# Optimization experiments

Hardware: AMD Instinct MI355X
Metric: run time of the kernel (lower is better)

## Reference

```python
import jax, jax.numpy as jnp
import numpy as np

B, N, M, K, D, DO = 4, 32768, 8192, 16, 128, 128


def setup_inputs() -> dict:
    key = jax.random.key(0)
    ks = jax.random.split(key, 8)
    return dict(
        xyz=jax.random.normal(ks[0], (B, N, 3), jnp.float32),
        x=jax.random.normal(ks[1], (B, D, N), jnp.float32),
        xyz_center=jax.random.normal(ks[2], (B, M, 3), jnp.float32),
        idx=jax.random.randint(ks[3], (B, M, K), 0, N, jnp.int32),
        alpha=jnp.ones((1,), jnp.float32),
        beta=jnp.ones((1,), jnp.float32),
        norm_radius=jnp.ones((1,), jnp.float32),
        w1=jax.random.normal(ks[4], (K, 3), jnp.float32) * 0.1,
        g1=jnp.ones((K,), jnp.float32),
        b1=jnp.zeros((K,), jnp.float32),
        w2=jax.random.normal(ks[5], (K, 2 * K), jnp.float32) * 0.1,
        g2=jnp.ones((K,), jnp.float32),
        b2=jnp.zeros((K,), jnp.float32),
        w3=jax.random.normal(ks[6], (K, 2 * K), jnp.float32) * 0.1,
        cv_w=jax.random.normal(ks[7], (DO, D, K), jnp.float32) * 0.02,
    )


def _inorm(t, g, b, eps=1e-5):
    # InstanceNorm2d: normalize each (batch, channel) plane over spatial dims (m, k)
    mu = t.mean(axis=(2, 3), keepdims=True)
    var = t.var(axis=(2, 3), keepdims=True)
    return (t - mu) * jax.lax.rsqrt(var + eps) * g[None, :, None, None] + b[None, :, None, None]


def reference(xyz, x, xyz_center, idx, alpha, beta, norm_radius, w1, g1, b1, w2, g2, b2, w3, cv_w):
    k = idx.shape[-1]
    gather = jax.vmap(lambda pts, i: pts[i])  # per-batch gather
    xyz_group = gather(xyz, idx)                      # b m k 3
    x_group = gather(jnp.swapaxes(x, 1, 2), idx)      # b m k d

    pts = xyz_group - xyz_center[:, :, None, :]       # b m k 3
    # dist computed on detached pts (torch .detach())
    dist = jnp.sqrt(jnp.sum(jnp.square(jax.lax.stop_gradient(pts)), -1))  # b m k
    mean_radius = dist.max(-1).mean()
    nr = norm_radius * 0.9 + mean_radius * 0.1        # EMA-updated radius (non-trainable)
    pts = pts / nr

    dw = jax.nn.sigmoid(-alpha * dist + beta)         # b m k
    s = dw.sum(-1, keepdims=True)
    s = s + (s == 0).astype(dw.dtype) + 1e-6
    dw = dw / s * k
    dw4 = dw[:, None, :, :]                           # b 1 m k

    ptsT = jnp.transpose(pts, (0, 3, 1, 2))           # b 3 m k
    mat = jax.nn.relu(_inorm(jnp.einsum('bcmk,oc->bomk', ptsT, w1), g1, b1))
    mp1 = jnp.broadcast_to((mat * dw4).max(-1, keepdims=True), mat.shape)
    mat = jax.nn.relu(_inorm(jnp.einsum('bcmk,oc->bomk', jnp.concatenate([mat, mp1], 1), w2), g2, b2))
    mp2 = jnp.broadcast_to((mat * dw4).max(-1, keepdims=True), mat.shape)
    mat = jax.nn.relu(jnp.einsum('bcmk,oc->bomk', jnp.concatenate([mat, mp2], 1), w3)) * dw4

    out = jnp.einsum('bmkd,bjmk->bdmj', x_group, mat)  # b d m k
    out = jnp.einsum('bdmj,odj->bom', out, cv_w)
    return out
```

## Files before the change

### kernel.cpp

```cpp
#include <hip/hip_runtime.h>
#include <hip/hip_bf16.h>

#define BB 4
#define NN 32768
#define MM 8192
#define KK 16
#define DD 128
#define DOUT 128
#define TT 2048

typedef unsigned short ushortT;
typedef unsigned int uintT;
typedef __attribute__((ext_vector_type(8))) short short8;
typedef __attribute__((ext_vector_type(4))) float f32x4;
typedef __attribute__((ext_vector_type(2))) float f32x2;

__device__ __forceinline__ ushortT f2bf(float f) {
  union { float f; uintT u; } v; v.f = f;
  uintT u = v.u;
  return (ushortT)((u + 0x7FFFu + ((u >> 16) & 1u)) >> 16);
}

#define ST_MAXD 0
#define ST_E1 16
#define ST_A1 160
#define ST_B1 224
#define ST_E2 288
#define ST_A2 416
#define ST_B2 480

__global__ __launch_bounds__(256) void kxT(const float* __restrict__ x, ushortT* __restrict__ xTb) {
  __shared__ float tile[32][33];
  const int b = blockIdx.z;
  const int n0 = blockIdx.x * 32, d0 = blockIdx.y * 32;
  const int tx = threadIdx.x, ty = threadIdx.y;
  const float* xp = x + (size_t)b * DD * NN;
  #pragma unroll
  for (int i = 0; i < 4; i++)
    tile[ty + i * 8][tx] = xp[(size_t)(d0 + ty + i * 8) * NN + n0 + tx];
  __syncthreads();
  ushortT* op = xTb + (size_t)b * NN * DD;
  #pragma unroll
  for (int i = 0; i < 4; i++)
    op[(size_t)(n0 + ty + i * 8) * DD + d0 + tx] = f2bf(tile[tx][ty + i * 8]);
}

__global__ __launch_bounds__(256) void kWb(const float* __restrict__ cw, ushortT* __restrict__ wb) {
  const int i = blockIdx.x * 256 + threadIdx.x;
  wb[i] = f2bf(cw[i]);
}

__global__ __launch_bounds__(256) void kpassA(const float* __restrict__ xyz,
    const float* __restrict__ xyzc, const int* __restrict__ idx,
    const float* __restrict__ w1, float* __restrict__ st, float4* __restrict__ pts4) {
  const int b = blockIdx.y;
  const int tid = threadIdx.x;
  const int mloc = tid >> 4, k = tid & 15;
  const int m = blockIdx.x * 16 + mloc;
  const int gi = (b * MM + m) * KK + k;
  const int n = idx[gi];
  const float cx = xyzc[(b * MM + m) * 3 + 0];
  const float cy = xyzc[(b * MM + m) * 3 + 1];
  const float cz = xyzc[(b * MM + m) * 3 + 2];
  const float* p = xyz + ((size_t)b * NN + n) * 3;
  const float px = p[0] - cx, py = p[1] - cy, pz = p[2] - cz;
  const float dist = sqrtf(px * px + py * py + pz * pz);
  pts4[gi] = (float4){px, py, pz, dist};
  float maxd = dist;
  maxd = fmaxf(maxd, __shfl_xor(maxd, 1));
  maxd = fmaxf(maxd, __shfl_xor(maxd, 2));
  maxd = fmaxf(maxd, __shfl_xor(maxd, 4));
  maxd = fmaxf(maxd, __shfl_xor(maxd, 8));
  __shared__ float red[16];
  __shared__ float wred[4][32];
  if (k == 0) red[mloc] = maxd;
  float vs[16], vq[16];
  #pragma unroll
  for (int o = 0; o < 16; o++) {
    float e = px * w1[3 * o] + py * w1[3 * o + 1] + pz * w1[3 * o + 2];
    vs[o] = e; vq[o] = e * e;
  }
  #pragma unroll
  for (int s = 1; s < 64; s <<= 1) {
    #pragma unroll
    for (int o = 0; o < 16; o++) {
      vs[o] += __shfl_xor(vs[o], s);
      vq[o] += __shfl_xor(vq[o], s);
    }
  }
  const int wv = tid >> 6, lane = tid & 63;
  if (lane == 0) {
    #pragma unroll
    for (int o = 0; o < 16; o++) { wred[wv][o] = vs[o]; wred[wv][16 + o] = vq[o]; }
  }
  __syncthreads();
  if (tid < 32) {
    float a = wred[0][tid] + wred[1][tid] + wred[2][tid] + wred[3][tid];
    atomicAdd(&st[ST_E1 + b * 32 + tid], a);
  }
  if (tid == 0) {
    float s = 0.f;
    #pragma unroll
    for (int i = 0; i < 16; i++) s += red[i];
    atomicAdd(&st[ST_MAXD], s);
  }
}

__global__ void kS1(const float* __restrict__ nrad, const float* __restrict__ g1,
                    const float* __restrict__ b1, float* __restrict__ st) {
  const int tid = threadIdx.x;
  if (tid >= 64) return;
  const float meanrad = st[ST_MAXD] / (float)(BB * MM);
  const float nr = nrad[0] * 0.9f + meanrad * 0.1f;
  const int b = tid >> 4, o = tid & 15;
  const float cnt = (float)(MM * KK);
  const float sum = st[ST_E1 + b * 32 + o];
  const float sq  = st[ST_E1 + b * 32 + 16 + o];
  const float mu = sum / cnt;
  float var = sq / cnt - mu * mu; var = fmaxf(var, 0.f);
  const float invs = rsqrtf(var + 1e-5f * nr * nr);
  const float a = invs * g1[o];
  st[ST_A1 + b * 16 + o] = a;
  st[ST_B1 + b * 16 + o] = b1[o] - mu * a;
}

__global__ __launch_bounds__(256) void kpassB(const float4* __restrict__ pts4,
    const float* __restrict__ alpha, const float* __restrict__ beta,
    const float* __restrict__ w1, const float* __restrict__ w2,
    float* __restrict__ st) {
  const int b = blockIdx.y;
  const int tid = threadIdx.x;
  __shared__ float wred[4][32];
  const int gi = b * MM * KK + blockIdx.x * 256 + tid;
  const float4 p4 = pts4[gi];
  const float px = p4.x, py = p4.y, pz = p4.z, dist = p4.w;
  float dwv = 1.f / (1.f + expf(alpha[0] * dist - beta[0]));
  float s = dwv;
  s += __shfl_xor(s, 1); s += __shfl_xor(s, 2); s += __shfl_xor(s, 4); s += __shfl_xor(s, 8);
  s = s + (s == 0.f ? 1.f : 0.f) + 1e-6f;
  dwv = dwv / s * 16.f;
  f32x2 v1[16];
  #pragma unroll
  for (int o = 0; o < 16; o++) {
    float e = px * w1[3 * o] + py * w1[3 * o + 1] + pz * w1[3 * o + 2];
    float v = e * st[ST_A1 + b * 16 + o] + st[ST_B1 + b * 16 + o];
    v = fmaxf(v, 0.f);
    float t = v * dwv;
    t = fmaxf(t, __shfl_xor(t, 1)); t = fmaxf(t, __shfl_xor(t, 2));
    t = fmaxf(t, __shfl_xor(t, 4)); t = fmaxf(t, __shfl_xor(t, 8));
    if (o & 1) { v1[o >> 1].y = v; v1[8 + (o >> 1)].y = t; }
    else       { v1[o >> 1].x = v; v1[8 + (o >> 1)].x = t; }
  }
  float vs[16], vq[16];
  #pragma unroll
  for (int o = 0; o < 16; o++) {
    f32x2 acc = {0.f, 0.f};
    #pragma unroll
    for (int cp = 0; cp < 16; cp++) {
      const f32x2 wv = *(const f32x2*)(w2 + o * 32 + 2 * cp);
      acc += v1[cp] * wv;
    }
    const float e = acc.x + acc.y;
    vs[o] = e; vq[o] = e * e;
  }
  #pragma unroll
  for (int s2 = 1; s2 < 64; s2 <<= 1) {
    #pragma unroll
    for (int o = 0; o < 16; o++) {
      vs[o] += __shfl_xor(vs[o], s2);
      vq[o] += __shfl_xor(vq[o], s2);
    }
  }
  const int wv = tid >> 6, lane = tid & 63;
  if (lane == 0) {
    #pragma unroll
    for (int o = 0; o < 16; o++) { wred[wv][o] = vs[o]; wred[wv][16 + o] = vq[o]; }
  }
  __syncthreads();
  if (tid < 32) {
    float a = wred[0][tid] + wred[1][tid] + wred[2][tid] + wred[3][tid];
    atomicAdd(&st[ST_E2 + b * 32 + tid], a);
  }
}

__global__ void kS2(const float* __restrict__ g2, const float* __restrict__ b2,
                    float* __restrict__ st) {
  const int tid = threadIdx.x;
  if (tid >= 64) return;
  const int b = tid >> 4, o = tid & 15;
  const float cnt = (float)(MM * KK);
  const float sum = st[ST_E2 + b * 32 + o];
  const float sq  = st[ST_E2 + b * 32 + 16 + o];
  const float mu = sum / cnt;
  float var = sq / cnt - mu * mu; var = fmaxf(var, 0.f);
  const float invs = rsqrtf(var + 1e-5f);
  const float a = invs * g2[o];
  st[ST_A2 + b * 16 + o] = a;
  st[ST_B2 + b * 16 + o] = b2[o] - mu * a;
}

__global__ __launch_bounds__(256, 6) void kMat3(const float* __restrict__ xyz,
    const float* __restrict__ xyzc, const int* __restrict__ idx,
    const float* __restrict__ alpha, const float* __restrict__ beta,
    const float* __restrict__ w1, const float* __restrict__ w2,
    const float* __restrict__ w3, const float* __restrict__ st,
    float* __restrict__ mat3g) {
  const int b = blockIdx.y;
  const int tid = threadIdx.x;
  const int mloc = tid >> 4, k1 = tid & 15;
  const int m = blockIdx.x * 16 + mloc;
  const int gi = (b * MM + m) * KK + k1;
  const int n = idx[gi];
  const float cx = xyzc[(b * MM + m) * 3 + 0];
  const float cy = xyzc[(b * MM + m) * 3 + 1];
  const float cz = xyzc[(b * MM + m) * 3 + 2];
  const float* p = xyz + ((size_t)b * NN + n) * 3;
  const float px = p[0] - cx, py = p[1] - cy, pz = p[2] - cz;
  const float dist = sqrtf(px * px + py * py + pz * pz);
  float dwv = 1.f / (1.f + expf(alpha[0] * dist - beta[0]));
  {
    float s = dwv;
    s += __shfl_xor(s, 1); s += __shfl_xor(s, 2); s += __shfl_xor(s, 4); s += __shfl_xor(s, 8);
    s = s + (s == 0.f ? 1.f : 0.f) + 1e-6f;
    dwv = dwv / s * 16.f;
  }
  f32x2 v1[16];
  #pragma unroll
  for (int o = 0; o < 16; o++) {
    float e = px * w1[3 * o] + py * w1[3 * o + 1] + pz * w1[3 * o + 2];
    float v = e * st[ST_A1 + b * 16 + o] + st[ST_B1 + b * 16 + o];
    v = fmaxf(v, 0.f);
    float t = v * dwv;
    t = fmaxf(t, __shfl_xor(t, 1)); t = fmaxf(t, __shfl_xor(t, 2));
    t = fmaxf(t, __shfl_xor(t, 4)); t = fmaxf(t, __shfl_xor(t, 8));
    if (o & 1) { v1[o >> 1].y = v; v1[8 + (o >> 1)].y = t; }
    else       { v1[o >> 1].x = v; v1[8 + (o >> 1)].x = t; }
  }
  float in2[16];
  #pragma unroll
  for (int o = 0; o < 16; o++) {
    f32x2 acc = {0.f, 0.f};
    #pragma unroll
    for (int cp = 0; cp < 16; cp++) {
      const f32x2 wv = *(const f32x2*)(w2 + o * 32 + 2 * cp);
      acc += v1[cp] * wv;
    }
    float v = (acc.x + acc.y) * st[ST_A2 + b * 16 + o] + st[ST_B2 + b * 16 + o];
    in2[o] = fmaxf(v, 0.f);
  }
  f32x2 v2[16];
  #pragma unroll
  for (int o = 0; o < 16; o++) {
    float t = in2[o] * dwv;
    t = fmaxf(t, __shfl_xor(t, 1)); t = fmaxf(t, __shfl_xor(t, 2));
    t = fmaxf(t, __shfl_xor(t, 4)); t = fmaxf(t, __shfl_xor(t, 8));
    if (o & 1) { v2[o >> 1].y = in2[o]; v2[8 + (o >> 1)].y = t; }
    else       { v2[o >> 1].x = in2[o]; v2[8 + (o >> 1)].x = t; }
  }
  float m3v[16];
  #pragma unroll
  for (int j = 0; j < 16; j++) {
    f32x2 acc = {0.f, 0.f};
    #pragma unroll
    for (int cp = 0; cp < 16; cp++) {
      const f32x2 wv = *(const f32x2*)(w3 + j * 32 + 2 * cp);
      acc += v2[cp] * wv;
    }
    m3v[j] = fmaxf(acc.x + acc.y, 0.f) * dwv;
  }
  const int swz1 = (k1 ^ (k1 >> 2)) & 3;
  float* m3w = mat3g + (((size_t)b * MM + blockIdx.x * 16) << 8) + tid * 16;
  #pragma unroll
  for (int q = 0; q < 4; q++)
    *(f32x4*)(m3w + ((q ^ swz1) << 2)) =
        (f32x4){m3v[4 * q], m3v[4 * q + 1], m3v[4 * q + 2], m3v[4 * q + 3]};
}

__global__ __launch_bounds__(512, 3) void kF2(const int* __restrict__ idx,
    const float* __restrict__ mat3g, const ushortT* __restrict__ xTb,
    ushortT* __restrict__ Aout) {
  __shared__ float mat3s[32 * 256];
  const int b = blockIdx.y;
  const int tid = threadIdx.x;
  const int m0 = blockIdx.x * 32;

  const int wid = __builtin_amdgcn_readfirstlane(tid >> 6);
  const int lane = tid & 63;
  const int mh = lane >> 5;
  const int dq = lane & 31;
  const int d0 = dq * 4;
  const ushortT* xb = xTb + (size_t)b * NN * DD + d0;

  uint2 xA[16], xB[16];

#define PREF(dst, gg) do {                                                 \
    const int* ib0 = idx + ((b * MM + m0 + (gg) * 16 + wid * 2) << 4);     \
    const int* ib1 = ib0 + 16;                                             \
    _Pragma("unroll")                                                      \
    for (int t = 0; t < 16; t++) {                                         \
      const int ke = ib0[t], ko = ib1[t];                                  \
      const uintT nn = (uintT)(mh ? ko : ke);                              \
      (dst)[t] = *(const uint2*)(xb + ((size_t)nn << 7));                  \
    }                                                                      \
  } while (0)

  PREF(xA, 0);

  {
    const f32x4* src = (const f32x4*)(mat3g + (((size_t)b * MM + m0) << 8));
    f32x4* dst = (f32x4*)mat3s;
    #pragma unroll
    for (int i = 0; i < 4; i++)
      dst[tid + i * 512] = src[tid + i * 512];
  }
  __syncthreads();

#define COMP(src, gg) do {                                                 \
    const float* m3base = &mat3s[((gg) * 16 + wid * 2 + mh) * 256];        \
    f32x2 a2[4][8];                                                        \
    _Pragma("unroll")                                                      \
    for (int d = 0; d < 4; d++)                                            \
      _Pragma("unroll")                                                    \
      for (int c = 0; c < 8; c++) a2[d][c] = (f32x2){0.f, 0.f};            \
    _Pragma("unroll")                                                      \
    for (int t = 0; t < 16; t++) {                                         \
      const int sw = (t ^ (t >> 2)) & 3;                                   \
      const uint2 xv = (src)[t];                                           \
      const f32x4 mq0 = *(const f32x4*)(m3base + t * 16 + ((0 ^ sw) << 2));\
      const f32x4 mq1 = *(const f32x4*)(m3base + t * 16 + ((1 ^ sw) << 2));\
      const f32x4 mq2 = *(const f32x4*)(m3base + t * 16 + ((2 ^ sw) << 2));\
      const f32x4 mq3 = *(const f32x4*)(m3base + t * 16 + ((3 ^ sw) << 2));\
      float xs[4];                                                         \
      xs[0] = __uint_as_float(xv.x << 16);                                 \
      xs[1] = __uint_as_float(xv.x & 0xFFFF0000u);                         \
      xs[2] = __uint_as_float(xv.y << 16);                                 \
      xs[3] = __uint_as_float(xv.y & 0xFFFF0000u);                         \
      f32x2 mp[8];                                                         \
      mp[0] = mq0.lo; mp[1] = mq0.hi;                                      \
      mp[2] = mq1.lo; mp[3] = mq1.hi;                                      \
      mp[4] = mq2.lo; mp[5] = mq2.hi;                                      \
      mp[6] = mq3.lo; mp[7] = mq3.hi;                                      \
      _Pragma("unroll")                                                    \
      for (int d = 0; d < 4; d++) {                                        \
        const float xd = xs[d];                                            \
        _Pragma("unroll")                                                  \
        for (int c = 0; c < 8; c++)                                        \
          a2[d][c] += mp[c] * xd;                                          \
      }                                                                    \
    }                                                                      \
    ushortT* aop = Aout + ((size_t)b * MM + m0 + (gg) * 16 + wid * 2 + mh) * TT + d0 * 16; \
    _Pragma("unroll")                                                      \
    for (int d = 0; d < 4; d++) {                                          \
      uintT u[8];                                                          \
      _Pragma("unroll")                                                    \
      for (int c = 0; c < 8; c++)                                          \
        u[c] = (uintT)f2bf(a2[d][c].x) | ((uintT)f2bf(a2[d][c].y) << 16);  \
      *(uint4*)(aop + d * 16)     = (uint4){u[0], u[1], u[2], u[3]};       \
      *(uint4*)(aop + d * 16 + 8) = (uint4){u[4], u[5], u[6], u[7]};       \
    }                                                                      \
  } while (0)

  PREF(xB, 1);
  COMP(xA, 0);
  COMP(xB, 1);

#undef PREF
#undef COMP
}

__global__ __launch_bounds__(512) void kgemm(const ushortT* __restrict__ Wb,
                                             const ushortT* __restrict__ Aout,
                                             float* __restrict__ out) {
  __shared__ ushortT At[128 * 40];
  __shared__ ushortT Bt[128 * 40];
  const int b = blockIdx.y;
  const int m0 = blockIdx.x * 128;
  const int tid = threadIdx.x;
  const int w = tid >> 6, l = tid & 63;
  const int ow = (w >> 2) * 64, mw = (w & 3) * 32;
  const int fr = l & 15, fg = l >> 4;
  f32x4 acc[4][2];
  #pragma unroll
  for (int i = 0; i < 4; i++)
    #pragma unroll
    for (int j = 0; j < 2; j++)
      acc[i][j] = (f32x4){0.f, 0.f, 0.f, 0.f};
  const int srow = tid >> 2, sk = (tid & 3) * 8;
  const ushortT* wp = Wb + srow * TT + sk;
  const ushortT* ap = Aout + ((size_t)b * MM + m0 + srow) * TT + sk;
  for (int k0 = 0; k0 < TT; k0 += 32) {
    uint4 wv = *(const uint4*)(wp + k0);
    uint4 av = *(const uint4*)(ap + k0);
    *(uint4*)&At[srow * 40 + sk] = wv;
    *(uint4*)&Bt[srow * 40 + sk] = av;
    __syncthreads();
    short8 a[4], bfrag[2];
    #pragma unroll
    for (int i = 0; i < 4; i++) a[i] = *(short8*)&At[(ow + i * 16 + fr) * 40 + fg * 8];
    #pragma unroll
    for (int j = 0; j < 2; j++) bfrag[j] = *(short8*)&Bt[(mw + j * 16 + fr) * 40 + fg * 8];
    #pragma unroll
    for (int i = 0; i < 4; i++)
      #pragma unroll
      for (int j = 0; j < 2; j++)
        acc[i][j] = __builtin_amdgcn_mfma_f32_16x16x32_bf16(a[i], bfrag[j], acc[i][j], 0, 0, 0);
    __syncthreads();
  }
  #pragma unroll
  for (int i = 0; i < 4; i++)
    #pragma unroll
    for (int j = 0; j < 2; j++)
      #pragma unroll
      for (int r = 0; r < 4; r++) {
        const int o = ow + i * 16 + fg * 4 + r;
        const int m = m0 + mw + j * 16 + fr;
        out[((size_t)b * DOUT + o) * MM + m] = acc[i][j][r];
      }
}

#define XTB_OFF 0
#define PTS_OFF 33554432
#define MAT3_OFF 33554432
#define AOUT_OFF 67108864
#define WB_OFF 201326592
#define ST_OFF 201850880

extern "C" void kernel_launch(void* const* d_in, const int* in_sizes, int n_in,
                              void* d_out, int out_size, void* d_ws, size_t ws_size,
                              hipStream_t stream) {
  const float* xyz  = (const float*)d_in[0];
  const float* x    = (const float*)d_in[1];
  const float* xyzc = (const float*)d_in[2];
  const int*   idx  = (const int*)d_in[3];
  const float* alpha = (const float*)d_in[4];
  const float* beta  = (const float*)d_in[5];
  const float* nrad  = (const float*)d_in[6];
  const float* w1 = (const float*)d_in[7];
  const float* g1 = (const float*)d_in[8];
  const float* b1 = (const float*)d_in[9];
  const float* w2 = (const float*)d_in[10];
  const float* g2 = (const float*)d_in[11];
  const float* b2 = (const float*)d_in[12];
  const float* w3 = (const float*)d_in[13];
  const float* cvw = (const float*)d_in[14];
  char* ws = (char*)d_ws;
  ushortT* xTb  = (ushortT*)(ws + XTB_OFF);
  float4*  pts4 = (float4*)(ws + PTS_OFF);
  float*   mat3g = (float*)(ws + MAT3_OFF);
  ushortT* Aout = (ushortT*)(ws + AOUT_OFF);
  ushortT* Wb   = (ushortT*)(ws + WB_OFF);
  float*   st   = (float*)(ws + ST_OFF);
  float* out = (float*)d_out;

  hipMemsetAsync(st, 0, 4096, stream);
  kxT<<<dim3(NN / 32, DD / 32, BB), dim3(32, 8), 0, stream>>>(x, xTb);
  kWb<<<dim3(DOUT * TT / 256), 256, 0, stream>>>(cvw, Wb);
  kpassA<<<dim3(MM / 16, BB), 256, 0, stream>>>(xyz, xyzc, idx, w1, st, pts4);
  kS1<<<1, 64, 0, stream>>>(nrad, g1, b1, st);
  kpassB<<<dim3(MM / 16, BB), 256, 0, stream>>>(pts4, alpha, beta, w1, w2, st);
  kS2<<<1, 64, 0, stream>>>(g2, b2, st);
  kMat3<<<dim3(MM / 16, BB), 256, 0, stream>>>(xyz, xyzc, idx, alpha, beta, w1, w2, w3, st, mat3g);
  kF2<<<dim3(MM / 32, BB), 512, 0, stream>>>(idx, mat3g, xTb, Aout);
  kgemm<<<dim3(MM / 128, BB), 512, 0, stream>>>(Wb, Aout, out);
}
```

Before: 236.2 us.

## Fuse mat3 MLP computation into gather-aggregate kernel via shared memory

Merges the kernel that computed the per-neighbor MLP weights (mat3) with the kernel that gathers features and aggregates them. mat3 now goes straight to LDS instead of being written to and read back from a global workspace, and the kernel reads precomputed pts4 (offsets plus distance) instead of re-gathering xyz. This removes one launch and the global round-trip of the mat3 buffer. In exchange, blocks shrink to 256 threads over 16 centers with lower occupancy hints, and the feature prefetch now overlaps with MLP compute, which raises register pressure.

```diff
diff --git a/kernel.cpp b/kernel.cpp
--- a/kernel.cpp
+++ b/kernel.cpp
@@ -199,24 +199,20 @@
   st[ST_B2 + b * 16 + o] = b2[o] - mu * a;
 }
 
-__global__ __launch_bounds__(256, 6) void kMat3(const float* __restrict__ xyz,
-    const float* __restrict__ xyzc, const int* __restrict__ idx,
+__global__ __launch_bounds__(256, 3) void kF1m(const float4* __restrict__ pts4,
+    const int* __restrict__ idx,
     const float* __restrict__ alpha, const float* __restrict__ beta,
-    const float* __restrict__ w1, const float* __restrict__ w2,
-    const float* __restrict__ w3, const float* __restrict__ st,
-    float* __restrict__ mat3g) {
+    const float* __restrict__ w1, const float* __restrict__ w2, const float* __restrict__ w3,
+    const float* __restrict__ st, const ushortT* __restrict__ xTb, ushortT* __restrict__ Aout) {
+  __shared__ float mat3s[16 * 256];
   const int b = blockIdx.y;
   const int tid = threadIdx.x;
+  const int m0 = blockIdx.x * 16;
+
   const int mloc = tid >> 4, k1 = tid & 15;
-  const int m = blockIdx.x * 16 + mloc;
-  const int gi = (b * MM + m) * KK + k1;
-  const int n = idx[gi];
-  const float cx = xyzc[(b * MM + m) * 3 + 0];
-  const float cy = xyzc[(b * MM + m) * 3 + 1];
-  const float cz = xyzc[(b * MM + m) * 3 + 2];
-  const float* p = xyz + ((size_t)b * NN + n) * 3;
-  const float px = p[0] - cx, py = p[1] - cy, pz = p[2] - cz;
-  const float dist = sqrtf(px * px + py * py + pz * pz);
+  const int gi = (b * MM + m0) * KK + tid;
+  const float4 p4 = pts4[gi];
+  const float px = p4.x, py = p4.y, pz = p4.z, dist = p4.w;
   float dwv = 1.f / (1.f + expf(alpha[0] * dist - beta[0]));
   {
     float s = dwv;
@@ -236,53 +232,6 @@
     if (o & 1) { v1[o >> 1].y = v; v1[8 + (o >> 1)].y = t; }
     else       { v1[o >> 1].x = v; v1[8 + (o >> 1)].x = t; }
   }
-  float in2[16];
-  #pragma unroll
-  for (int o = 0; o < 16; o++) {
-    f32x2 acc = {0.f, 0.f};
-    #pragma unroll
-    for (int cp = 0; cp < 16; cp++) {
-      const f32x2 wv = *(const f32x2*)(w2 + o * 32 + 2 * cp);
-      acc += v1[cp] * wv;
-    }
-    float v = (acc.x + acc.y) * st[ST_A2 + b * 16 + o] + st[ST_B2 + b * 16 + o];
-    in2[o] = fmaxf(v, 0.f);
-  }
-  f32x2 v2[16];
-  #pragma unroll
-  for (int o = 0; o < 16; o++) {
-    float t = in2[o] * dwv;
-    t = fmaxf(t, __shfl_xor(t, 1)); t = fmaxf(t, __shfl_xor(t, 2));
-    t = fmaxf(t, __shfl_xor(t, 4)); t = fmaxf(t, __shfl_xor(t, 8));
-    if (o & 1) { v2[o >> 1].y = in2[o]; v2[8 + (o >> 1)].y = t; }
-    else       { v2[o >> 1].x = in2[o]; v2[8 + (o >> 1)].x = t; }
-  }
-  float m3v[16];
-  #pragma unroll
-  for (int j = 0; j < 16; j++) {
-    f32x2 acc = {0.f, 0.f};
-    #pragma unroll
-    for (int cp = 0; cp < 16; cp++) {
-      const f32x2 wv = *(const f32x2*)(w3 + j * 32 + 2 * cp);
-      acc += v2[cp] * wv;
-    }
-    m3v[j] = fmaxf(acc.x + acc.y, 0.f) * dwv;
-  }
-  const int swz1 = (k1 ^ (k1 >> 2)) & 3;
-  float* m3w = mat3g + (((size_t)b * MM + blockIdx.x * 16) << 8) + tid * 16;
-  #pragma unroll
-  for (int q = 0; q < 4; q++)
-    *(f32x4*)(m3w + ((q ^ swz1) << 2)) =
-        (f32x4){m3v[4 * q], m3v[4 * q + 1], m3v[4 * q + 2], m3v[4 * q + 3]};
-}
-
-__global__ __launch_bounds__(512, 3) void kF2(const int* __restrict__ idx,
-    const float* __restrict__ mat3g, const ushortT* __restrict__ xTb,
-    ushortT* __restrict__ Aout) {
-  __shared__ float mat3s[32 * 256];
-  const int b = blockIdx.y;
-  const int tid = threadIdx.x;
-  const int m0 = blockIdx.x * 32;
 
   const int wid = __builtin_amdgcn_readfirstlane(tid >> 6);
   const int lane = tid & 63;
@@ -293,8 +242,8 @@
 
   uint2 xA[16], xB[16];
 
-#define PREF(dst, gg) do {                                                 \
-    const int* ib0 = idx + ((b * MM + m0 + (gg) * 16 + wid * 2) << 4);     \
+#define PREF(dst, p) do {                                                  \
+    const int* ib0 = idx + ((b * MM + m0 + (p) * 2) << 4);                 \
     const int* ib1 = ib0 + 16;                                             \
     _Pragma("unroll")                                                      \
     for (int t = 0; t < 16; t++) {                                         \
@@ -304,19 +253,52 @@
     }                                                                      \
   } while (0)
 
-  PREF(xA, 0);
+  PREF(xA, wid);
 
   {
-    const f32x4* src = (const f32x4*)(mat3g + (((size_t)b * MM + m0) << 8));
-    f32x4* dst = (f32x4*)mat3s;
-    #pragma unroll
-    for (int i = 0; i < 4; i++)
-      dst[tid + i * 512] = src[tid + i * 512];
+    float in2[16];
+    #pragma unroll
+    for (int o = 0; o < 16; o++) {
+      f32x2 acc = {0.f, 0.f};
+      #pragma unroll
+      for (int cp = 0; cp < 16; cp++) {
+        const f32x2 wv = *(const f32x2*)(w2 + o * 32 + 2 * cp);
+        acc += v1[cp] * wv;
+      }
+      float v = (acc.x + acc.y) * st[ST_A2 + b * 16 + o] + st[ST_B2 + b * 16 + o];
+      in2[o] = fmaxf(v, 0.f);
+    }
+    f32x2 v2[16];
+    #pragma unroll
+    for (int o = 0; o < 16; o++) {
+      float t = in2[o] * dwv;
+      t = fmaxf(t, __shfl_xor(t, 1)); t = fmaxf(t, __shfl_xor(t, 2));
+      t = fmaxf(t, __shfl_xor(t, 4)); t = fmaxf(t, __shfl_xor(t, 8));
+      if (o & 1) { v2[o >> 1].y = in2[o]; v2[8 + (o >> 1)].y = t; }
+      else       { v2[o >> 1].x = in2[o]; v2[8 + (o >> 1)].x = t; }
+    }
+    float m3v[16];
+    #pragma unroll
+    for (int j = 0; j < 16; j++) {
+      f32x2 acc = {0.f, 0.f};
+      #pragma unroll
+      for (int cp = 0; cp < 16; cp++) {
+        const f32x2 wv = *(const f32x2*)(w3 + j * 32 + 2 * cp);
+        acc += v2[cp] * wv;
+      }
+      m3v[j] = fmaxf(acc.x + acc.y, 0.f) * dwv;
+    }
+    const int swz1 = (k1 ^ (k1 >> 2)) & 3;
+    float* m3w = &mat3s[mloc * 256 + k1 * 16];
+    #pragma unroll
+    for (int q = 0; q < 4; q++)
+      *(f32x4*)(m3w + ((q ^ swz1) << 2)) =
+          (f32x4){m3v[4 * q], m3v[4 * q + 1], m3v[4 * q + 2], m3v[4 * q + 3]};
   }
   __syncthreads();
 
-#define COMP(src, gg) do {                                                 \
-    const float* m3base = &mat3s[((gg) * 16 + wid * 2 + mh) * 256];        \
+#define COMP(src, p) do {                                                  \
+    const float* m3base = &mat3s[((p) * 2 + mh) * 256];                    \
     f32x2 a2[4][8];                                                        \
     _Pragma("unroll")                                                      \
     for (int d = 0; d < 4; d++)                                            \
@@ -348,7 +330,7 @@
           a2[d][c] += mp[c] * xd;                                          \
       }                                                                    \
     }                                                                      \
-    ushortT* aop = Aout + ((size_t)b * MM + m0 + (gg) * 16 + wid * 2 + mh) * TT + d0 * 16; \
+    ushortT* aop = Aout + ((size_t)b * MM + m0 + (p) * 2 + mh) * TT + d0 * 16; \
     _Pragma("unroll")                                                      \
     for (int d = 0; d < 4; d++) {                                          \
       uintT u[8];                                                          \
@@ -360,9 +342,9 @@
     }                                                                      \
   } while (0)
 
-  PREF(xB, 1);
-  COMP(xA, 0);
-  COMP(xB, 1);
+  PREF(xB, wid + 4);
+  COMP(xA, wid);
+  COMP(xB, wid + 4);
 
 #undef PREF
 #undef COMP
@@ -420,7 +402,6 @@
 
 #define XTB_OFF 0
 #define PTS_OFF 33554432
-#define MAT3_OFF 33554432
 #define AOUT_OFF 67108864
 #define WB_OFF 201326592
 #define ST_OFF 201850880
@@ -446,7 +427,6 @@
   char* ws = (char*)d_ws;
   ushortT* xTb  = (ushortT*)(ws + XTB_OFF);
   float4*  pts4 = (float4*)(ws + PTS_OFF);
-  float*   mat3g = (float*)(ws + MAT3_OFF);
   ushortT* Aout = (ushortT*)(ws + AOUT_OFF);
   ushortT* Wb   = (ushortT*)(ws + WB_OFF);
   float*   st   = (float*)(ws + ST_OFF);
@@ -459,7 +439,6 @@
   kS1<<<1, 64, 0, stream>>>(nrad, g1, b1, st);
   kpassB<<<dim3(MM / 16, BB), 256, 0, stream>>>(pts4, alpha, beta, w1, w2, st);
   kS2<<<1, 64, 0, stream>>>(g2, b2, st);
-  kMat3<<<dim3(MM / 16, BB), 256, 0, stream>>>(xyz, xyzc, idx, alpha, beta, w1, w2, w3, st, mat3g);
-  kF2<<<dim3(MM / 32, BB), 512, 0, stream>>>(idx, mat3g, xTb, Aout);
+  kF1m<<<dim3(MM / 16, BB), 256, 0, stream>>>(pts4, idx, alpha, beta, w1, w2, w3, st, xTb, Aout);
   kgemm<<<dim3(MM / 128, BB), 512, 0, stream>>>(Wb, Aout, out);
 }
```

New measurement: 215.9 us. -8.6%, faster.
